# Kernel tuning notes

Measured on AMD Instinct MI355X. Metric: run time of the kernel, lower is better.

The kernel has to match this reference:

```python
import jax, jax.numpy as jnp
import numpy as np

N_NODES = 50000


def gcn_conv(x, src, dst, W, b, n):
    # PyG GCNConv: h = x @ W; out[i] = sum_j norm_ij * h[j] + b, with added self-loops
    h = x @ W  # [N, out]
    deg = jax.ops.segment_sum(jnp.ones_like(dst, dtype=h.dtype), dst, num_segments=n)
    inv_sqrt_deg = jnp.where(deg > 0, jax.lax.rsqrt(deg), 0.0)  # [N]
    coeff = inv_sqrt_deg[src] * inv_sqrt_deg[dst]  # [E]
    msg = h[src] * coeff[:, None]  # [E, out] gather (memory-bound)
    out = jax.ops.segment_sum(msg, dst, num_segments=n)  # scatter-add
    return out + b


def setup_inputs() -> dict:
    key = jax.random.key(0)
    ks = jax.random.split(key, 8)
    n, e, c_in, c_hid, c_out = N_NODES, 800000, 128, 128, 64
    x = jax.random.normal(ks[0], (n, c_in), dtype=jnp.float32)
    edge_index = jax.random.randint(ks[1], (2, e), 0, n, dtype=jnp.int64)
    # Glorot-ish scaled weights
    W1 = jax.random.normal(ks[2], (c_in, c_hid), dtype=jnp.float32) / np.sqrt(c_in)
    b1 = jnp.zeros((c_hid,), dtype=jnp.float32)
    W2 = jax.random.normal(ks[3], (c_hid, c_out), dtype=jnp.float32) / np.sqrt(c_hid)
    b2 = jnp.zeros((c_out,), dtype=jnp.float32)
    lin_W = jax.random.normal(ks[4], (2 * c_out, c_out), dtype=jnp.float32) / np.sqrt(2 * c_out)
    lin_b = jnp.zeros((c_out,), dtype=jnp.float32)
    return {"x": x, "edge_index": edge_index, "W1": W1, "b1": b1,
            "W2": W2, "b2": b2, "lin_W": lin_W, "lin_b": lin_b}


def reference(x, edge_index, W1, b1, W2, b2, lin_W, lin_b):
    n = x.shape[0]
    # add self-loops (as GCNConv does by default)
    loops = jnp.arange(n, dtype=edge_index.dtype)
    src = jnp.concatenate([edge_index[0], loops])
    dst = jnp.concatenate([edge_index[1], loops])

    def branch(x):
        h = jax.nn.relu(gcn_conv(x, src, dst, W1, b1, n))
        # dropout: identity in eval mode (training=False)
        return gcn_conv(h, src, dst, W2, b2, n)

    x1 = branch(x)
    x2 = branch(x)
    # FusionMethod == 'Concat'
    fused = jnp.concatenate([x1, x2], axis=1) @ lin_W + lin_b
    return jax.nn.log_softmax(fused, axis=1)
```

## Files before the change

kernel.cpp:

```cpp
#include <hip/hip_runtime.h>


#define CIN  128
#define CHID 128
#define COUT 64
#define BCAP_SH 13
#define BINCHUNK 2048
#define CELLCAP 32
#define ENTCAP  5120

typedef short v8s __attribute__((ext_vector_type(8)));
typedef float v4f __attribute__((ext_vector_type(4)));

static __device__ __forceinline__ unsigned short f2bf(float f) {
    unsigned int u = __float_as_uint(f);
    unsigned int r = (u + 0x7fffu + ((u >> 16) & 1u)) >> 16;
    return (unsigned short)r;
}
static __device__ __forceinline__ float bflo(unsigned int u) {
    return __uint_as_float(u << 16);
}
static __device__ __forceinline__ float bfhi(unsigned int u) {
    return __uint_as_float(u & 0xffff0000u);
}
static __device__ __forceinline__ unsigned int pk2(float a, float b) {
    return (unsigned int)f2bf(a) | ((unsigned int)f2bf(b) << 16);
}

__global__ __launch_bounds__(256) void bin_wprep_kernel(
        const int* __restrict__ src, const int* __restrict__ dst,
        int* __restrict__ cnt, unsigned int* __restrict__ binned, int E, int nchunk,
        const float* __restrict__ W1, const float* __restrict__ W2,
        const float* __restrict__ b2, const float* __restrict__ linW,
        const float* __restrict__ linb, unsigned short* __restrict__ Wt1,
        unsigned short* __restrict__ Wt2, float* __restrict__ bp) {
    int bb = blockIdx.x;
    int t = threadIdx.x;
    if (bb < nchunk) {
        __shared__ int h[256];
        __shared__ int cur[256];
        h[t] = 0;
        __syncthreads();
        int e0 = bb * BINCHUNK;
        int e1 = e0 + BINCHUNK; if (e1 > E) e1 = E;
        for (int e = e0 + t; e < e1; e += 256)
            atomicAdd(&h[dst[e] >> 8], 1);
        __syncthreads();
        int c = h[t];
        cnt[bb * 256 + t] = c < CELLCAP ? c : CELLCAP;
        cur[t] = 0;
        __syncthreads();
        for (int e = e0 + t; e < e1; e += 256) {
            int d = dst[e];
            int b = d >> 8;
            int pos = atomicAdd(&cur[b], 1);
            if (pos < CELLCAP)
                binned[((size_t)(bb * 256 + b)) * CELLCAP + pos] =
                    (unsigned int)src[e] | (((unsigned int)d & 255u) << 16);
        }
    } else {
        int wb = bb - nchunk;
        if (wb < CHID) {
            if (t < 128) {
                Wt1[wb * CIN + t] = f2bf(W1[t * CHID + wb]);
                if (t < COUT) {
                    float acc = 0.f;
#pragma unroll 8
                    for (int k = 0; k < COUT; ++k) {
                        float wsv = linW[k * COUT + t] + linW[(k + COUT) * COUT + t];
                        acc = fmaf(W2[wb * COUT + k], wsv, acc);
                    }
                    Wt2[t * CHID + wb] = f2bf(acc);
                }
            }
        } else {
            if (t < COUT) {
                float acc = 0.f;
#pragma unroll 8
                for (int k = 0; k < COUT; ++k) {
                    float wsv = linW[k * COUT + t] + linW[(k + COUT) * COUT + t];
                    acc = fmaf(b2[k], wsv, acc);
                }
                bp[t] = acc + linb[t];
            }
        }
    }
}

__global__ __launch_bounds__(512) void csr_gemm1_kernel(
        const unsigned int* __restrict__ binned, const int* __restrict__ cnt,
        int nchunk, int nbkt,
        int2* __restrict__ rowpair, float* __restrict__ inv,
        unsigned short* __restrict__ ebuf16,
        const float* __restrict__ x, const unsigned short* __restrict__ Wt1,
        unsigned short* __restrict__ h1t, int n) {
    int t = threadIdx.x;
    if ((int)blockIdx.x < nbkt) {
        int b = blockIdx.x;
        __shared__ int cc[512];
        __shared__ int ps[512];
        __shared__ unsigned int ent[ENTCAP];
        __shared__ int h[256];
        __shared__ int s2[256];
        int v = (t < nchunk) ? cnt[t * 256 + b] : 0;
        cc[t] = v;
        ps[t] = v;
        __syncthreads();
        for (int off = 1; off < 512; off <<= 1) {
            int u = (t >= off) ? ps[t - off] : 0;
            __syncthreads();
            ps[t] += u;
            __syncthreads();
        }
        int total = ps[511];
        if (total > ENTCAP) total = ENTCAP;
        if (t < nchunk && v > 0) {
            int basei = ps[t] - v;
            const unsigned int* cell = binned + ((size_t)(t * 256 + b)) * CELLCAP;
            for (int i = 0; i < v; ++i)
                if (basei + i < ENTCAP) ent[basei + i] = cell[i];
        }
        if (t < 256) h[t] = 0;
        __syncthreads();
        for (int i = t; i < total; i += 512)
            atomicAdd(&h[ent[i] >> 16], 1);
        __syncthreads();
        int myc = (t < 256) ? h[t] : 0;
        if (t < 256) s2[t] = myc;
        __syncthreads();
        for (int off = 1; off < 256; off <<= 1) {
            int u = (t >= off && t < 256) ? s2[t - off] : 0;
            __syncthreads();
            if (t < 256) s2[t] += u;
            __syncthreads();
        }
        int base = b << BCAP_SH;
        if (t < 256) {
            int excl = s2[t] - myc;
            int node = (b << 8) + t;
            if (node < n) {
                rowpair[node] = make_int2(base + excl, base + excl + myc);
                inv[node] = rsqrtf((float)(myc + 1));
            }
            h[t] = base + excl;
        }
        __syncthreads();
        for (int i = t; i < total; i += 512) {
            unsigned int e = ent[i];
            int pos = atomicAdd(&h[e >> 16], 1);
            ebuf16[pos] = (unsigned short)(e & 0xffffu);
        }
    } else {
        int bid = blockIdx.x - nbkt;
        int lane = t & 63, wave = t >> 6;
        int quad = lane >> 4, r16 = lane & 15;
        int row0 = (bid * 8 + wave) * 16;
        if (row0 >= n) return;
        int arow = row0 + r16;
        if (arow >= n) arow = n - 1;
        size_t n32 = (size_t)n * 32;

        v4f acc[8];
#pragma unroll
        for (int c = 0; c < 8; ++c) acc[c] = (v4f){0.f, 0.f, 0.f, 0.f};
#pragma unroll
        for (int kc = 0; kc < 4; ++kc) {
            const float4* ap = (const float4*)(x + (size_t)arow * 128 + kc * 32 + quad * 8);
            float4 a0 = ap[0], a1 = ap[1];
            v8s af;
            af[0] = (short)f2bf(a0.x); af[1] = (short)f2bf(a0.y);
            af[2] = (short)f2bf(a0.z); af[3] = (short)f2bf(a0.w);
            af[4] = (short)f2bf(a1.x); af[5] = (short)f2bf(a1.y);
            af[6] = (short)f2bf(a1.z); af[7] = (short)f2bf(a1.w);
#pragma unroll
            for (int ct = 0; ct < 8; ++ct) {
                v8s bf = *(const v8s*)(Wt1 + (size_t)(ct * 16 + r16) * 128 + kc * 32 + quad * 8);
                acc[ct] = __builtin_amdgcn_mfma_f32_16x16x32_bf16(af, bf, acc[ct], 0, 0, 0);
            }
        }
#pragma unroll
        for (int ct = 0; ct < 8; ++ct) {
            int col = ct * 16 + r16;
            int pl = col >> 5, d = col & 31;
#pragma unroll
            for (int i = 0; i < 4; ++i) {
                int orow = row0 + quad * 4 + i;
                if (orow < n)
                    h1t[(size_t)pl * n32 + (size_t)orow * 32 + d] = f2bf(acc[ct][i]);
            }
        }
    }
}

__global__ __launch_bounds__(256) void agg1_slice_kernel(
        const unsigned short* __restrict__ h1t,
        const unsigned short* __restrict__ ebuf16,
        const int2* __restrict__ rowpair,
        const float* __restrict__ inv,
        const float* __restrict__ b1,
        unsigned int* __restrict__ agg1b,
        int n) {
    int b = blockIdx.x;
    int xcd = b & 7;
    int slice = xcd >> 1;
    int sub = xcd & 1;
    int grp = b >> 3;
    int wid = threadIdx.x >> 6;
    int lane = threadIdx.x & 63;
    int g = lane >> 3, s = lane & 7;
    const uint2* __restrict__ plane = (const uint2*)(h1t + (size_t)slice * n * 32);

    int node = (grp * 2 + sub) * 32 + wid * 8 + g;
    int cnode = node < n ? node : n - 1;
    int2 rp = rowpair[cnode];
    int beg = rp.x, len = rp.y - rp.x;
    int m = len < 64 ? len : 64;
    uint2 usl = plane[(size_t)cnode * 8 + s];
    float wd = inv[cnode];
    float4 bv = ((const float4*)b1)[slice * 8 + s];

    int kmax = (m + 1) & ~1;
    float a0 = 0.f, a1 = 0.f, a2 = 0.f, a3 = 0.f;
    int g8 = g << 3;
    int eid = 0;
    for (int k = 0; k < kmax; k += 2) {
        if ((k & 7) == 0) eid = (int)ebuf16[beg + k + s];
        int sa = __shfl(eid, g8 + (k & 7), 64);
        int sb = __shfl(eid, g8 + (k & 7) + 1, 64);
        sb = (k + 1 < m) ? sb : cnode;
        float iva = inv[sa], ivb = inv[sb];
        uint2 ua = plane[(size_t)sa * 8 + s];
        uint2 ub = plane[(size_t)sb * 8 + s];
        a0 = fmaf(iva, bflo(ua.x), a0); a1 = fmaf(iva, bfhi(ua.x), a1);
        a2 = fmaf(iva, bflo(ua.y), a2); a3 = fmaf(iva, bfhi(ua.y), a3);
        a0 = fmaf(ivb, bflo(ub.x), a0); a1 = fmaf(ivb, bfhi(ub.x), a1);
        a2 = fmaf(ivb, bflo(ub.y), a2); a3 = fmaf(ivb, bfhi(ub.y), a3);
    }
    if (len > 64) {
        for (int k = 64; k < len; ++k) {
            int sid = (int)ebuf16[beg + k];
            float iv2 = inv[sid];
            uint2 u = plane[(size_t)sid * 8 + s];
            a0 = fmaf(iv2, bflo(u.x), a0); a1 = fmaf(iv2, bfhi(u.x), a1);
            a2 = fmaf(iv2, bflo(u.y), a2); a3 = fmaf(iv2, bfhi(u.y), a3);
        }
    }
    float c2 = (1.0f - (float)(kmax - m)) * wd;
    a0 = fmaf(c2, bflo(usl.x), a0); a1 = fmaf(c2, bfhi(usl.x), a1);
    a2 = fmaf(c2, bflo(usl.y), a2); a3 = fmaf(c2, bfhi(usl.y), a3);
    float o0 = fmaxf(fmaf(wd, a0, bv.x), 0.f);
    float o1 = fmaxf(fmaf(wd, a1, bv.y), 0.f);
    float o2 = fmaxf(fmaf(wd, a2, bv.z), 0.f);
    float o3 = fmaxf(fmaf(wd, a3, bv.w), 0.f);
    if (node < n) {
        uint2 w; w.x = pk2(o0, o1); w.y = pk2(o2, o3);
        ((uint2*)agg1b)[(size_t)node * 32 + slice * 8 + s] = w;
    }
}

__global__ __launch_bounds__(256) void gemm2_kernel(const unsigned short* __restrict__ A,
                                                    const unsigned short* __restrict__ Wt,
                                                    const float* __restrict__ inv,
                                                    unsigned short* __restrict__ h2t, int n) {
    int lane = threadIdx.x & 63;
    int wave = threadIdx.x >> 6;
    int quad = lane >> 4, r16 = lane & 15;
    int row0 = (blockIdx.x * 4 + wave) * 16;
    if (row0 >= n) return;
    int arow = row0 + r16;
    if (arow >= n) arow = n - 1;

    v4f acc[4];
#pragma unroll
    for (int c = 0; c < 4; ++c) acc[c] = (v4f){0.f, 0.f, 0.f, 0.f};
#pragma unroll
    for (int kc = 0; kc < 4; ++kc) {
        v8s af = *(const v8s*)(A + (size_t)arow * 128 + kc * 32 + quad * 8);
#pragma unroll
        for (int ct = 0; ct < 4; ++ct) {
            v8s bf = *(const v8s*)(Wt + (size_t)(ct * 16 + r16) * 128 + kc * 32 + quad * 8);
            acc[ct] = __builtin_amdgcn_mfma_f32_16x16x32_bf16(af, bf, acc[ct], 0, 0, 0);
        }
    }
    float4 iv = ((const float4*)(inv + row0))[quad];
#pragma unroll
    for (int ct = 0; ct < 4; ++ct) {
#pragma unroll
        for (int i = 0; i < 4; ++i) {
            int orow = row0 + quad * 4 + i;
            if (orow < n) {
                float sc = (i == 0) ? iv.x : (i == 1) ? iv.y : (i == 2) ? iv.z : iv.w;
                h2t[(size_t)orow * 64 + ct * 16 + r16] = f2bf(acc[ct][i] * sc);
            }
        }
    }
}

__global__ __launch_bounds__(256) void agg2_softmax_kernel(
        const unsigned short* __restrict__ h2t,
        const unsigned short* __restrict__ ebuf16,
        const int2* __restrict__ rowpair,
        const float* __restrict__ inv,
        const float* __restrict__ bp,
        float* __restrict__ outp, int n) {
    int wid = threadIdx.x >> 6;
    int lane = threadIdx.x & 63;
    int g = lane >> 3, s = lane & 7;
    int node = blockIdx.x * 32 + wid * 8 + g;
    int cnode = node < n ? node : n - 1;
    int2 rp = rowpair[cnode];
    int beg = rp.x, len = rp.y - rp.x;
    int m = len < 64 ? len : 64;
    const uint4* __restrict__ rows = (const uint4*)h2t;
    uint4 usl = rows[(size_t)cnode * 8 + s];
    float wd = inv[cnode];

    int kmax = (m + 1) & ~1;
    float a0 = 0.f, a1 = 0.f, a2 = 0.f, a3 = 0.f;
    float a4 = 0.f, a5 = 0.f, a6 = 0.f, a7 = 0.f;
    int g8 = g << 3;
    int eid = 0;
    for (int k = 0; k < kmax; k += 2) {
        if ((k & 7) == 0) eid = (int)ebuf16[beg + k + s];
        int sa = __shfl(eid, g8 + (k & 7), 64);
        int sb = __shfl(eid, g8 + (k & 7) + 1, 64);
        sb = (k + 1 < m) ? sb : cnode;
        uint4 ua = rows[(size_t)sa * 8 + s];
        uint4 ub = rows[(size_t)sb * 8 + s];
        a0 += bflo(ua.x); a1 += bfhi(ua.x); a2 += bflo(ua.y); a3 += bfhi(ua.y);
        a4 += bflo(ua.z); a5 += bfhi(ua.z); a6 += bflo(ua.w); a7 += bfhi(ua.w);
        a0 += bflo(ub.x); a1 += bfhi(ub.x); a2 += bflo(ub.y); a3 += bfhi(ub.y);
        a4 += bflo(ub.z); a5 += bfhi(ub.z); a6 += bflo(ub.w); a7 += bfhi(ub.w);
    }
    if (len > 64) {
        for (int k = 64; k < len; ++k) {
            int sid = (int)ebuf16[beg + k];
            uint4 u = rows[(size_t)sid * 8 + s];
            a0 += bflo(u.x); a1 += bfhi(u.x); a2 += bflo(u.y); a3 += bfhi(u.y);
            a4 += bflo(u.z); a5 += bfhi(u.z); a6 += bflo(u.w); a7 += bfhi(u.w);
        }
    }
    float c2 = 1.0f - (float)(kmax - m);
    a0 = fmaf(c2, bflo(usl.x), a0); a1 = fmaf(c2, bfhi(usl.x), a1);
    a2 = fmaf(c2, bflo(usl.y), a2); a3 = fmaf(c2, bfhi(usl.y), a3);
    a4 = fmaf(c2, bflo(usl.z), a4); a5 = fmaf(c2, bfhi(usl.z), a5);
    a6 = fmaf(c2, bflo(usl.w), a6); a7 = fmaf(c2, bfhi(usl.w), a7);
    float4 bpa = ((const float4*)bp)[s * 2];
    float4 bpb = ((const float4*)bp)[s * 2 + 1];
    float f0 = fmaf(wd, a0, bpa.x), f1 = fmaf(wd, a1, bpa.y);
    float f2 = fmaf(wd, a2, bpa.z), f3 = fmaf(wd, a3, bpa.w);
    float f4 = fmaf(wd, a4, bpb.x), f5 = fmaf(wd, a5, bpb.y);
    float f6 = fmaf(wd, a6, bpb.z), f7 = fmaf(wd, a7, bpb.w);
    float mx = fmaxf(fmaxf(fmaxf(f0, f1), fmaxf(f2, f3)),
                     fmaxf(fmaxf(f4, f5), fmaxf(f6, f7)));
    mx = fmaxf(mx, __shfl_xor(mx, 1, 64));
    mx = fmaxf(mx, __shfl_xor(mx, 2, 64));
    mx = fmaxf(mx, __shfl_xor(mx, 4, 64));
    float sum = expf(f0 - mx) + expf(f1 - mx) + expf(f2 - mx) + expf(f3 - mx)
              + expf(f4 - mx) + expf(f5 - mx) + expf(f6 - mx) + expf(f7 - mx);
    sum += __shfl_xor(sum, 1, 64);
    sum += __shfl_xor(sum, 2, 64);
    sum += __shfl_xor(sum, 4, 64);
    float ls = mx + logf(sum);
    if (node < n) {
        float4 w0 = make_float4(f0 - ls, f1 - ls, f2 - ls, f3 - ls);
        float4 w1 = make_float4(f4 - ls, f5 - ls, f6 - ls, f7 - ls);
        ((float4*)outp)[(size_t)node * 16 + s * 2]     = w0;
        ((float4*)outp)[(size_t)node * 16 + s * 2 + 1] = w1;
    }
}

static inline size_t align16(size_t x) { return (x + 15) & ~(size_t)15; }

extern "C" void kernel_launch(void* const* d_in, const int* in_sizes, int n_in,
                              void* d_out, int out_size, void* d_ws, size_t ws_size,
                              hipStream_t stream) {
    const float* x    = (const float*)d_in[0];
    const int*   eidx = (const int*)d_in[1];
    const float* W1   = (const float*)d_in[2];
    const float* b1   = (const float*)d_in[3];
    const float* W2   = (const float*)d_in[4];
    const float* b2   = (const float*)d_in[5];
    const float* linW = (const float*)d_in[6];
    const float* linb = (const float*)d_in[7];
    float* out = (float*)d_out;

    const int n = in_sizes[0] / CIN;
    const int E = in_sizes[1] / 2;
    const int* src = eidx;
    const int* dst = eidx + E;
    const int NBKT = (n + 255) >> 8;
    const int NCHUNK = (E + BINCHUNK - 1) / BINCHUNK;

    char* ws = (char*)d_ws;
    size_t off = 0;
    int2*  rowpair = (int2*)(ws + off);  off = align16(off + (size_t)n * 8);
    float* inv     = (float*)(ws + off); off = align16(off + (size_t)n * 4);
    int*   cnt     = (int*)(ws + off);   off = align16(off + (size_t)NCHUNK * 256 * 4);
    unsigned short* Wt1 = (unsigned short*)(ws + off); off = align16(off + (size_t)CHID * CIN * 2);
    unsigned short* Wt2 = (unsigned short*)(ws + off); off = align16(off + (size_t)COUT * CHID * 2);
    float* bp      = (float*)(ws + off); off = align16(off + (size_t)COUT * 4);
    unsigned int* binned = (unsigned int*)(ws + off);
    off = align16(off + (size_t)NCHUNK * 256 * CELLCAP * 4);
    unsigned short* ebuf16 = (unsigned short*)(ws + off);
    off = align16(off + (size_t)256 * (1 << BCAP_SH) * 2);
    unsigned short* h1t   = (unsigned short*)(ws + off); off = align16(off + (size_t)n * CHID * 2);
    unsigned int*   agg1b = (unsigned int*)(ws + off);   off = align16(off + (size_t)n * CHID * 2);
    unsigned short* h2t   = (unsigned short*)(ws + off); off = align16(off + (size_t)n * COUT * 2);

    bin_wprep_kernel<<<NCHUNK + CHID + 1, 256, 0, stream>>>(
        src, dst, cnt, binned, E, NCHUNK, W1, W2, b2, linW, linb, Wt1, Wt2, bp);

    const int G1B = (n + 127) / 128;
    csr_gemm1_kernel<<<NBKT + G1B, 512, 0, stream>>>(
        binned, cnt, NCHUNK, NBKT, rowpair, inv, ebuf16, x, Wt1, h1t, n);

    const int NG1 = (n + 63) / 64;
    agg1_slice_kernel<<<NG1 * 8, 256, 0, stream>>>(h1t, ebuf16, rowpair, inv, b1, agg1b, n);

    gemm2_kernel<<<(n + 63) / 64, 256, 0, stream>>>((const unsigned short*)agg1b, Wt2, inv, h2t, n);

    agg2_softmax_kernel<<<(n + 31) / 32, 256, 0, stream>>>(h2t, ebuf16, rowpair, inv, bp, out, n);
}
```

Baseline: 191.6 us.

## Merge all stages into one cooperative persistent kernel with grid syncs

Replaces the five separate kernel launches with a single cooperative mega-kernel. Each stage runs as a grid-strided loop, and stages are separated by grid-wide barriers. The CSR build no longer stages entries in a large shared buffer and reads binned cells straight from global memory. Aggregation 2 is split from the log-softmax pass, which now goes through the output buffer. The aim is to remove launch overhead and the tail gaps between kernels. In exchange it adds several grid syncs, occupancy limits from the persistent grid, and an extra round trip of the output through global memory.

```diff
diff --git a/kernel.cpp b/kernel.cpp
--- a/kernel.cpp
+++ b/kernel.cpp
@@ -1,4 +1,7 @@
 #include <hip/hip_runtime.h>
+#include <hip/hip_cooperative_groups.h>
+
+namespace cg = cooperative_groups;
 
 
 #define CIN  128
@@ -7,7 +10,6 @@
 #define BCAP_SH 13
 #define BINCHUNK 2048
 #define CELLCAP 32
-#define ENTCAP  5120
 
 typedef short v8s __attribute__((ext_vector_type(8)));
 typedef float v4f __attribute__((ext_vector_type(4)));
@@ -27,346 +29,345 @@
     return (unsigned int)f2bf(a) | ((unsigned int)f2bf(b) << 16);
 }
 
-__global__ __launch_bounds__(256) void bin_wprep_kernel(
-        const int* __restrict__ src, const int* __restrict__ dst,
-        int* __restrict__ cnt, unsigned int* __restrict__ binned, int E, int nchunk,
-        const float* __restrict__ W1, const float* __restrict__ W2,
-        const float* __restrict__ b2, const float* __restrict__ linW,
-        const float* __restrict__ linb, unsigned short* __restrict__ Wt1,
-        unsigned short* __restrict__ Wt2, float* __restrict__ bp) {
-    int bb = blockIdx.x;
-    int t = threadIdx.x;
-    if (bb < nchunk) {
-        __shared__ int h[256];
-        __shared__ int cur[256];
-        h[t] = 0;
-        __syncthreads();
-        int e0 = bb * BINCHUNK;
-        int e1 = e0 + BINCHUNK; if (e1 > E) e1 = E;
-        for (int e = e0 + t; e < e1; e += 256)
-            atomicAdd(&h[dst[e] >> 8], 1);
-        __syncthreads();
-        int c = h[t];
-        cnt[bb * 256 + t] = c < CELLCAP ? c : CELLCAP;
-        cur[t] = 0;
-        __syncthreads();
-        for (int e = e0 + t; e < e1; e += 256) {
-            int d = dst[e];
-            int b = d >> 8;
-            int pos = atomicAdd(&cur[b], 1);
-            if (pos < CELLCAP)
-                binned[((size_t)(bb * 256 + b)) * CELLCAP + pos] =
-                    (unsigned int)src[e] | (((unsigned int)d & 255u) << 16);
-        }
-    } else {
-        int wb = bb - nchunk;
-        if (wb < CHID) {
-            if (t < 128) {
-                Wt1[wb * CIN + t] = f2bf(W1[t * CHID + wb]);
-                if (t < COUT) {
-                    float acc = 0.f;
+struct MP {
+    const int* src; const int* dst;
+    const float* W1; const float* b1; const float* W2; const float* b2;
+    const float* linW; const float* linb; const float* x;
+    int* cnt; unsigned int* binned;
+    unsigned short* Wt1; unsigned short* Wt2; float* bp;
+    int2* rowpair; float* inv; unsigned short* ebuf16;
+    unsigned short* h1t; unsigned short* agg1b; unsigned short* h2t;
+    float* out;
+    int E, n, nchunk, nbkt;
+};
+
+__global__ __launch_bounds__(256, 4) void mega_kernel(MP p) {
+    cg::grid_group gg = cg::this_grid();
+    __shared__ int shA[256];
+    __shared__ int shB[256];
+    const int t = threadIdx.x;
+    const int nb = gridDim.x;
+    const int lane = t & 63;
+    const int wid = t >> 6;
+    const size_t n32 = (size_t)p.n * 32;
+
+    for (int u = blockIdx.x; u < p.nchunk + CHID + 1; u += nb) {
+        if (u < p.nchunk) {
+            shA[t] = 0;
+            __syncthreads();
+            int e0 = u * BINCHUNK;
+            int e1 = e0 + BINCHUNK; if (e1 > p.E) e1 = p.E;
+            for (int e = e0 + t; e < e1; e += 256)
+                atomicAdd(&shA[p.dst[e] >> 8], 1);
+            __syncthreads();
+            int c = shA[t];
+            p.cnt[u * 256 + t] = c < CELLCAP ? c : CELLCAP;
+            shB[t] = 0;
+            __syncthreads();
+            for (int e = e0 + t; e < e1; e += 256) {
+                int d = p.dst[e];
+                int b = d >> 8;
+                int pos = atomicAdd(&shB[b], 1);
+                if (pos < CELLCAP)
+                    p.binned[((size_t)(u * 256 + b)) * CELLCAP + pos] =
+                        (unsigned int)p.src[e] | (((unsigned int)d & 255u) << 16);
+            }
+            __syncthreads();
+        } else {
+            int wb = u - p.nchunk;
+            if (wb < CHID) {
+                if (t < 128) {
+                    p.Wt1[wb * CIN + t] = f2bf(p.W1[t * CHID + wb]);
+                    if (t < COUT) {
+                        float acc = 0.f;
 #pragma unroll 8
-                    for (int k = 0; k < COUT; ++k) {
-                        float wsv = linW[k * COUT + t] + linW[(k + COUT) * COUT + t];
-                        acc = fmaf(W2[wb * COUT + k], wsv, acc);
+                        for (int k = 0; k < COUT; ++k) {
+                            float wsv = p.linW[k * COUT + t] + p.linW[(k + COUT) * COUT + t];
+                            acc = fmaf(p.W2[wb * COUT + k], wsv, acc);
+                        }
+                        p.Wt2[t * CHID + wb] = f2bf(acc);
                     }
-                    Wt2[t * CHID + wb] = f2bf(acc);
-                }
-            }
-        } else {
-            if (t < COUT) {
+                }
+            } else if (t < COUT) {
                 float acc = 0.f;
 #pragma unroll 8
                 for (int k = 0; k < COUT; ++k) {
-                    float wsv = linW[k * COUT + t] + linW[(k + COUT) * COUT + t];
-                    acc = fmaf(b2[k], wsv, acc);
-                }
-                bp[t] = acc + linb[t];
-            }
-        }
-    }
-}
-
-__global__ __launch_bounds__(512) void csr_gemm1_kernel(
-        const unsigned int* __restrict__ binned, const int* __restrict__ cnt,
-        int nchunk, int nbkt,
-        int2* __restrict__ rowpair, float* __restrict__ inv,
-        unsigned short* __restrict__ ebuf16,
-        const float* __restrict__ x, const unsigned short* __restrict__ Wt1,
-        unsigned short* __restrict__ h1t, int n) {
-    int t = threadIdx.x;
-    if ((int)blockIdx.x < nbkt) {
-        int b = blockIdx.x;
-        __shared__ int cc[512];
-        __shared__ int ps[512];
-        __shared__ unsigned int ent[ENTCAP];
-        __shared__ int h[256];
-        __shared__ int s2[256];
-        int v = (t < nchunk) ? cnt[t * 256 + b] : 0;
-        cc[t] = v;
-        ps[t] = v;
-        __syncthreads();
-        for (int off = 1; off < 512; off <<= 1) {
-            int u = (t >= off) ? ps[t - off] : 0;
-            __syncthreads();
-            ps[t] += u;
-            __syncthreads();
-        }
-        int total = ps[511];
-        if (total > ENTCAP) total = ENTCAP;
-        if (t < nchunk && v > 0) {
-            int basei = ps[t] - v;
-            const unsigned int* cell = binned + ((size_t)(t * 256 + b)) * CELLCAP;
-            for (int i = 0; i < v; ++i)
-                if (basei + i < ENTCAP) ent[basei + i] = cell[i];
-        }
-        if (t < 256) h[t] = 0;
-        __syncthreads();
-        for (int i = t; i < total; i += 512)
-            atomicAdd(&h[ent[i] >> 16], 1);
-        __syncthreads();
-        int myc = (t < 256) ? h[t] : 0;
-        if (t < 256) s2[t] = myc;
+                    float wsv = p.linW[k * COUT + t] + p.linW[(k + COUT) * COUT + t];
+                    acc = fmaf(p.b2[k], wsv, acc);
+                }
+                p.bp[t] = acc + p.linb[t];
+            }
+        }
+    }
+    gg.sync();
+
+    for (int b = blockIdx.x; b < p.nbkt; b += nb) {
+        shA[t] = 0;
+        __syncthreads();
+        for (int c = t; c < p.nchunk; c += 256) {
+            int cc = p.cnt[c * 256 + b];
+            const unsigned int* cell = p.binned + ((size_t)(c * 256 + b)) * CELLCAP;
+            for (int i = 0; i < cc; ++i)
+                atomicAdd(&shA[cell[i] >> 16], 1);
+        }
+        __syncthreads();
+        int myc = shA[t];
+        shB[t] = myc;
         __syncthreads();
         for (int off = 1; off < 256; off <<= 1) {
-            int u = (t >= off && t < 256) ? s2[t - off] : 0;
-            __syncthreads();
-            if (t < 256) s2[t] += u;
+            int v = (t >= off) ? shB[t - off] : 0;
+            __syncthreads();
+            shB[t] += v;
             __syncthreads();
         }
         int base = b << BCAP_SH;
-        if (t < 256) {
-            int excl = s2[t] - myc;
-            int node = (b << 8) + t;
-            if (node < n) {
-                rowpair[node] = make_int2(base + excl, base + excl + myc);
-                inv[node] = rsqrtf((float)(myc + 1));
-            }
-            h[t] = base + excl;
-        }
-        __syncthreads();
-        for (int i = t; i < total; i += 512) {
-            unsigned int e = ent[i];
-            int pos = atomicAdd(&h[e >> 16], 1);
-            ebuf16[pos] = (unsigned short)(e & 0xffffu);
-        }
-    } else {
-        int bid = blockIdx.x - nbkt;
-        int lane = t & 63, wave = t >> 6;
+        int excl = shB[t] - myc;
+        int node = (b << 8) + t;
+        if (node < p.n) {
+            p.rowpair[node] = make_int2(base + excl, base + excl + myc);
+            p.inv[node] = rsqrtf((float)(myc + 1));
+        }
+        __syncthreads();
+        shA[t] = base + excl;
+        __syncthreads();
+        for (int c = t; c < p.nchunk; c += 256) {
+            int cc = p.cnt[c * 256 + b];
+            const unsigned int* cell = p.binned + ((size_t)(c * 256 + b)) * CELLCAP;
+            for (int i = 0; i < cc; ++i) {
+                unsigned int e = cell[i];
+                int pos = atomicAdd(&shA[e >> 16], 1);
+                p.ebuf16[pos] = (unsigned short)(e & 0xffffu);
+            }
+        }
+        __syncthreads();
+    }
+    gg.sync();
+
+    {
         int quad = lane >> 4, r16 = lane & 15;
-        int row0 = (bid * 8 + wave) * 16;
-        if (row0 >= n) return;
-        int arow = row0 + r16;
-        if (arow >= n) arow = n - 1;
-        size_t n32 = (size_t)n * 32;
-
-        v4f acc[8];
-#pragma unroll
-        for (int c = 0; c < 8; ++c) acc[c] = (v4f){0.f, 0.f, 0.f, 0.f};
-#pragma unroll
-        for (int kc = 0; kc < 4; ++kc) {
-            const float4* ap = (const float4*)(x + (size_t)arow * 128 + kc * 32 + quad * 8);
-            float4 a0 = ap[0], a1 = ap[1];
-            v8s af;
-            af[0] = (short)f2bf(a0.x); af[1] = (short)f2bf(a0.y);
-            af[2] = (short)f2bf(a0.z); af[3] = (short)f2bf(a0.w);
-            af[4] = (short)f2bf(a1.x); af[5] = (short)f2bf(a1.y);
-            af[6] = (short)f2bf(a1.z); af[7] = (short)f2bf(a1.w);
+        int nunits = (p.n + 63) >> 6;
+        for (int u = blockIdx.x; u < nunits; u += nb) {
+            int row0 = u * 64 + wid * 16;
+            if (row0 >= p.n) continue;
+            int arow = row0 + r16;
+            if (arow >= p.n) arow = p.n - 1;
+            v4f acc[8];
+#pragma unroll
+            for (int c = 0; c < 8; ++c) acc[c] = (v4f){0.f, 0.f, 0.f, 0.f};
+#pragma unroll
+            for (int kc = 0; kc < 4; ++kc) {
+                const float4* ap = (const float4*)(p.x + (size_t)arow * 128 + kc * 32 + quad * 8);
+                float4 a0 = ap[0], a1 = ap[1];
+                v8s af;
+                af[0] = (short)f2bf(a0.x); af[1] = (short)f2bf(a0.y);
+                af[2] = (short)f2bf(a0.z); af[3] = (short)f2bf(a0.w);
+                af[4] = (short)f2bf(a1.x); af[5] = (short)f2bf(a1.y);
+                af[6] = (short)f2bf(a1.z); af[7] = (short)f2bf(a1.w);
+#pragma unroll
+                for (int ct = 0; ct < 8; ++ct) {
+                    v8s bf = *(const v8s*)(p.Wt1 + (size_t)(ct * 16 + r16) * 128 + kc * 32 + quad * 8);
+                    acc[ct] = __builtin_amdgcn_mfma_f32_16x16x32_bf16(af, bf, acc[ct], 0, 0, 0);
+                }
+            }
+            float4 iv = ((const float4*)(p.inv + row0))[quad];
 #pragma unroll
             for (int ct = 0; ct < 8; ++ct) {
-                v8s bf = *(const v8s*)(Wt1 + (size_t)(ct * 16 + r16) * 128 + kc * 32 + quad * 8);
-                acc[ct] = __builtin_amdgcn_mfma_f32_16x16x32_bf16(af, bf, acc[ct], 0, 0, 0);
-            }
-        }
-#pragma unroll
-        for (int ct = 0; ct < 8; ++ct) {
-            int col = ct * 16 + r16;
-            int pl = col >> 5, d = col & 31;
-#pragma unroll
-            for (int i = 0; i < 4; ++i) {
-                int orow = row0 + quad * 4 + i;
-                if (orow < n)
-                    h1t[(size_t)pl * n32 + (size_t)orow * 32 + d] = f2bf(acc[ct][i]);
-            }
-        }
-    }
-}
-
-__global__ __launch_bounds__(256) void agg1_slice_kernel(
-        const unsigned short* __restrict__ h1t,
-        const unsigned short* __restrict__ ebuf16,
-        const int2* __restrict__ rowpair,
-        const float* __restrict__ inv,
-        const float* __restrict__ b1,
-        unsigned int* __restrict__ agg1b,
-        int n) {
-    int b = blockIdx.x;
-    int xcd = b & 7;
-    int slice = xcd >> 1;
-    int sub = xcd & 1;
-    int grp = b >> 3;
-    int wid = threadIdx.x >> 6;
-    int lane = threadIdx.x & 63;
-    int g = lane >> 3, s = lane & 7;
-    const uint2* __restrict__ plane = (const uint2*)(h1t + (size_t)slice * n * 32);
-
-    int node = (grp * 2 + sub) * 32 + wid * 8 + g;
-    int cnode = node < n ? node : n - 1;
-    int2 rp = rowpair[cnode];
-    int beg = rp.x, len = rp.y - rp.x;
-    int m = len < 64 ? len : 64;
-    uint2 usl = plane[(size_t)cnode * 8 + s];
-    float wd = inv[cnode];
-    float4 bv = ((const float4*)b1)[slice * 8 + s];
-
-    int kmax = (m + 1) & ~1;
-    float a0 = 0.f, a1 = 0.f, a2 = 0.f, a3 = 0.f;
-    int g8 = g << 3;
-    int eid = 0;
-    for (int k = 0; k < kmax; k += 2) {
-        if ((k & 7) == 0) eid = (int)ebuf16[beg + k + s];
-        int sa = __shfl(eid, g8 + (k & 7), 64);
-        int sb = __shfl(eid, g8 + (k & 7) + 1, 64);
-        sb = (k + 1 < m) ? sb : cnode;
-        float iva = inv[sa], ivb = inv[sb];
-        uint2 ua = plane[(size_t)sa * 8 + s];
-        uint2 ub = plane[(size_t)sb * 8 + s];
-        a0 = fmaf(iva, bflo(ua.x), a0); a1 = fmaf(iva, bfhi(ua.x), a1);
-        a2 = fmaf(iva, bflo(ua.y), a2); a3 = fmaf(iva, bfhi(ua.y), a3);
-        a0 = fmaf(ivb, bflo(ub.x), a0); a1 = fmaf(ivb, bfhi(ub.x), a1);
-        a2 = fmaf(ivb, bflo(ub.y), a2); a3 = fmaf(ivb, bfhi(ub.y), a3);
-    }
-    if (len > 64) {
-        for (int k = 64; k < len; ++k) {
-            int sid = (int)ebuf16[beg + k];
-            float iv2 = inv[sid];
-            uint2 u = plane[(size_t)sid * 8 + s];
-            a0 = fmaf(iv2, bflo(u.x), a0); a1 = fmaf(iv2, bfhi(u.x), a1);
-            a2 = fmaf(iv2, bflo(u.y), a2); a3 = fmaf(iv2, bfhi(u.y), a3);
-        }
-    }
-    float c2 = (1.0f - (float)(kmax - m)) * wd;
-    a0 = fmaf(c2, bflo(usl.x), a0); a1 = fmaf(c2, bfhi(usl.x), a1);
-    a2 = fmaf(c2, bflo(usl.y), a2); a3 = fmaf(c2, bfhi(usl.y), a3);
-    float o0 = fmaxf(fmaf(wd, a0, bv.x), 0.f);
-    float o1 = fmaxf(fmaf(wd, a1, bv.y), 0.f);
-    float o2 = fmaxf(fmaf(wd, a2, bv.z), 0.f);
-    float o3 = fmaxf(fmaf(wd, a3, bv.w), 0.f);
-    if (node < n) {
-        uint2 w; w.x = pk2(o0, o1); w.y = pk2(o2, o3);
-        ((uint2*)agg1b)[(size_t)node * 32 + slice * 8 + s] = w;
-    }
-}
-
-__global__ __launch_bounds__(256) void gemm2_kernel(const unsigned short* __restrict__ A,
-                                                    const unsigned short* __restrict__ Wt,
-                                                    const float* __restrict__ inv,
-                                                    unsigned short* __restrict__ h2t, int n) {
-    int lane = threadIdx.x & 63;
-    int wave = threadIdx.x >> 6;
-    int quad = lane >> 4, r16 = lane & 15;
-    int row0 = (blockIdx.x * 4 + wave) * 16;
-    if (row0 >= n) return;
-    int arow = row0 + r16;
-    if (arow >= n) arow = n - 1;
-
-    v4f acc[4];
-#pragma unroll
-    for (int c = 0; c < 4; ++c) acc[c] = (v4f){0.f, 0.f, 0.f, 0.f};
-#pragma unroll
-    for (int kc = 0; kc < 4; ++kc) {
-        v8s af = *(const v8s*)(A + (size_t)arow * 128 + kc * 32 + quad * 8);
-#pragma unroll
-        for (int ct = 0; ct < 4; ++ct) {
-            v8s bf = *(const v8s*)(Wt + (size_t)(ct * 16 + r16) * 128 + kc * 32 + quad * 8);
-            acc[ct] = __builtin_amdgcn_mfma_f32_16x16x32_bf16(af, bf, acc[ct], 0, 0, 0);
-        }
-    }
-    float4 iv = ((const float4*)(inv + row0))[quad];
-#pragma unroll
-    for (int ct = 0; ct < 4; ++ct) {
-#pragma unroll
-        for (int i = 0; i < 4; ++i) {
-            int orow = row0 + quad * 4 + i;
-            if (orow < n) {
-                float sc = (i == 0) ? iv.x : (i == 1) ? iv.y : (i == 2) ? iv.z : iv.w;
-                h2t[(size_t)orow * 64 + ct * 16 + r16] = f2bf(acc[ct][i] * sc);
-            }
-        }
-    }
-}
-
-__global__ __launch_bounds__(256) void agg2_softmax_kernel(
-        const unsigned short* __restrict__ h2t,
-        const unsigned short* __restrict__ ebuf16,
-        const int2* __restrict__ rowpair,
-        const float* __restrict__ inv,
-        const float* __restrict__ bp,
-        float* __restrict__ outp, int n) {
-    int wid = threadIdx.x >> 6;
-    int lane = threadIdx.x & 63;
-    int g = lane >> 3, s = lane & 7;
-    int node = blockIdx.x * 32 + wid * 8 + g;
-    int cnode = node < n ? node : n - 1;
-    int2 rp = rowpair[cnode];
-    int beg = rp.x, len = rp.y - rp.x;
-    int m = len < 64 ? len : 64;
-    const uint4* __restrict__ rows = (const uint4*)h2t;
-    uint4 usl = rows[(size_t)cnode * 8 + s];
-    float wd = inv[cnode];
-
-    int kmax = (m + 1) & ~1;
-    float a0 = 0.f, a1 = 0.f, a2 = 0.f, a3 = 0.f;
-    float a4 = 0.f, a5 = 0.f, a6 = 0.f, a7 = 0.f;
-    int g8 = g << 3;
-    int eid = 0;
-    for (int k = 0; k < kmax; k += 2) {
-        if ((k & 7) == 0) eid = (int)ebuf16[beg + k + s];
-        int sa = __shfl(eid, g8 + (k & 7), 64);
-        int sb = __shfl(eid, g8 + (k & 7) + 1, 64);
-        sb = (k + 1 < m) ? sb : cnode;
-        uint4 ua = rows[(size_t)sa * 8 + s];
-        uint4 ub = rows[(size_t)sb * 8 + s];
-        a0 += bflo(ua.x); a1 += bfhi(ua.x); a2 += bflo(ua.y); a3 += bfhi(ua.y);
-        a4 += bflo(ua.z); a5 += bfhi(ua.z); a6 += bflo(ua.w); a7 += bfhi(ua.w);
-        a0 += bflo(ub.x); a1 += bfhi(ub.x); a2 += bflo(ub.y); a3 += bfhi(ub.y);
-        a4 += bflo(ub.z); a5 += bfhi(ub.z); a6 += bflo(ub.w); a7 += bfhi(ub.w);
-    }
-    if (len > 64) {
-        for (int k = 64; k < len; ++k) {
-            int sid = (int)ebuf16[beg + k];
-            uint4 u = rows[(size_t)sid * 8 + s];
-            a0 += bflo(u.x); a1 += bfhi(u.x); a2 += bflo(u.y); a3 += bfhi(u.y);
-            a4 += bflo(u.z); a5 += bfhi(u.z); a6 += bflo(u.w); a7 += bfhi(u.w);
-        }
-    }
-    float c2 = 1.0f - (float)(kmax - m);
-    a0 = fmaf(c2, bflo(usl.x), a0); a1 = fmaf(c2, bfhi(usl.x), a1);
-    a2 = fmaf(c2, bflo(usl.y), a2); a3 = fmaf(c2, bfhi(usl.y), a3);
-    a4 = fmaf(c2, bflo(usl.z), a4); a5 = fmaf(c2, bfhi(usl.z), a5);
-    a6 = fmaf(c2, bflo(usl.w), a6); a7 = fmaf(c2, bfhi(usl.w), a7);
-    float4 bpa = ((const float4*)bp)[s * 2];
-    float4 bpb = ((const float4*)bp)[s * 2 + 1];
-    float f0 = fmaf(wd, a0, bpa.x), f1 = fmaf(wd, a1, bpa.y);
-    float f2 = fmaf(wd, a2, bpa.z), f3 = fmaf(wd, a3, bpa.w);
-    float f4 = fmaf(wd, a4, bpb.x), f5 = fmaf(wd, a5, bpb.y);
-    float f6 = fmaf(wd, a6, bpb.z), f7 = fmaf(wd, a7, bpb.w);
-    float mx = fmaxf(fmaxf(fmaxf(f0, f1), fmaxf(f2, f3)),
-                     fmaxf(fmaxf(f4, f5), fmaxf(f6, f7)));
-    mx = fmaxf(mx, __shfl_xor(mx, 1, 64));
-    mx = fmaxf(mx, __shfl_xor(mx, 2, 64));
-    mx = fmaxf(mx, __shfl_xor(mx, 4, 64));
-    float sum = expf(f0 - mx) + expf(f1 - mx) + expf(f2 - mx) + expf(f3 - mx)
-              + expf(f4 - mx) + expf(f5 - mx) + expf(f6 - mx) + expf(f7 - mx);
-    sum += __shfl_xor(sum, 1, 64);
-    sum += __shfl_xor(sum, 2, 64);
-    sum += __shfl_xor(sum, 4, 64);
-    float ls = mx + logf(sum);
-    if (node < n) {
-        float4 w0 = make_float4(f0 - ls, f1 - ls, f2 - ls, f3 - ls);
-        float4 w1 = make_float4(f4 - ls, f5 - ls, f6 - ls, f7 - ls);
-        ((float4*)outp)[(size_t)node * 16 + s * 2]     = w0;
-        ((float4*)outp)[(size_t)node * 16 + s * 2 + 1] = w1;
+                int col = ct * 16 + r16;
+                int pl = col >> 5, d = col & 31;
+#pragma unroll
+                for (int i = 0; i < 4; ++i) {
+                    int orow = row0 + quad * 4 + i;
+                    if (orow < p.n) {
+                        float sc = (i == 0) ? iv.x : (i == 1) ? iv.y : (i == 2) ? iv.z : iv.w;
+                        p.h1t[(size_t)pl * n32 + (size_t)orow * 32 + d] = f2bf(acc[ct][i] * sc);
+                    }
+                }
+            }
+        }
+    }
+    gg.sync();
+
+    {
+        int g = lane >> 3, s = lane & 7;
+        int g8 = g << 3;
+        int nunits = ((p.n + 63) >> 6) * 8;
+        for (int u = blockIdx.x; u < nunits; u += nb) {
+            int xcd = u & 7, slice = xcd >> 1, sub = xcd & 1, grp = u >> 3;
+            const uint2* plane = (const uint2*)(p.h1t + (size_t)slice * p.n * 32);
+            int node = (grp * 2 + sub) * 32 + wid * 8 + g;
+            int cnode = node < p.n ? node : p.n - 1;
+            int2 rp = p.rowpair[cnode];
+            int beg = rp.x, len = rp.y - rp.x;
+            int m = len < 64 ? len : 64;
+            uint2 usl = plane[(size_t)cnode * 8 + s];
+            float wd = p.inv[cnode];
+            float4 bv = ((const float4*)p.b1)[slice * 8 + s];
+            int kmax = (m + 3) & ~3;
+            float a0 = 0.f, a1 = 0.f, a2 = 0.f, a3 = 0.f;
+            int eid = 0;
+            for (int k = 0; k < kmax; k += 4) {
+                if ((k & 7) == 0) eid = (int)p.ebuf16[beg + k + s];
+                int i0 = __shfl(eid, g8 + (k & 7) + 0, 64);
+                int i1 = __shfl(eid, g8 + (k & 7) + 1, 64);
+                int i2 = __shfl(eid, g8 + (k & 7) + 2, 64);
+                int i3 = __shfl(eid, g8 + (k & 7) + 3, 64);
+                i0 = (k     < m) ? i0 : cnode;
+                i1 = (k + 1 < m) ? i1 : cnode;
+                i2 = (k + 2 < m) ? i2 : cnode;
+                i3 = (k + 3 < m) ? i3 : cnode;
+                uint2 u0 = plane[(size_t)i0 * 8 + s];
+                uint2 u1 = plane[(size_t)i1 * 8 + s];
+                uint2 u2 = plane[(size_t)i2 * 8 + s];
+                uint2 u3 = plane[(size_t)i3 * 8 + s];
+                a0 += bflo(u0.x); a1 += bfhi(u0.x); a2 += bflo(u0.y); a3 += bfhi(u0.y);
+                a0 += bflo(u1.x); a1 += bfhi(u1.x); a2 += bflo(u1.y); a3 += bfhi(u1.y);
+                a0 += bflo(u2.x); a1 += bfhi(u2.x); a2 += bflo(u2.y); a3 += bfhi(u2.y);
+                a0 += bflo(u3.x); a1 += bfhi(u3.x); a2 += bflo(u3.y); a3 += bfhi(u3.y);
+            }
+            if (len > 64) {
+                for (int k = 64; k < len; ++k) {
+                    int sid = (int)p.ebuf16[beg + k];
+                    uint2 uu = plane[(size_t)sid * 8 + s];
+                    a0 += bflo(uu.x); a1 += bfhi(uu.x); a2 += bflo(uu.y); a3 += bfhi(uu.y);
+                }
+            }
+            float cc = 1.0f - (float)(kmax - m);
+            a0 = fmaf(cc, bflo(usl.x), a0); a1 = fmaf(cc, bfhi(usl.x), a1);
+            a2 = fmaf(cc, bflo(usl.y), a2); a3 = fmaf(cc, bfhi(usl.y), a3);
+            float o0 = fmaxf(fmaf(wd, a0, bv.x), 0.f);
+            float o1 = fmaxf(fmaf(wd, a1, bv.y), 0.f);
+            float o2 = fmaxf(fmaf(wd, a2, bv.z), 0.f);
+            float o3 = fmaxf(fmaf(wd, a3, bv.w), 0.f);
+            if (node < p.n) {
+                uint2 w; w.x = pk2(o0, o1); w.y = pk2(o2, o3);
+                ((uint2*)p.agg1b)[(size_t)node * 32 + slice * 8 + s] = w;
+            }
+        }
+    }
+    gg.sync();
+
+    {
+        int quad = lane >> 4, r16 = lane & 15;
+        int nunits = (p.n + 63) >> 6;
+        for (int u = blockIdx.x; u < nunits; u += nb) {
+            int row0 = u * 64 + wid * 16;
+            if (row0 >= p.n) continue;
+            int arow = row0 + r16;
+            if (arow >= p.n) arow = p.n - 1;
+            v4f acc[4];
+#pragma unroll
+            for (int c = 0; c < 4; ++c) acc[c] = (v4f){0.f, 0.f, 0.f, 0.f};
+#pragma unroll
+            for (int kc = 0; kc < 4; ++kc) {
+                v8s af = *(const v8s*)(p.agg1b + (size_t)arow * 128 + kc * 32 + quad * 8);
+#pragma unroll
+                for (int ct = 0; ct < 4; ++ct) {
+                    v8s bf = *(const v8s*)(p.Wt2 + (size_t)(ct * 16 + r16) * 128 + kc * 32 + quad * 8);
+                    acc[ct] = __builtin_amdgcn_mfma_f32_16x16x32_bf16(af, bf, acc[ct], 0, 0, 0);
+                }
+            }
+            float4 iv = ((const float4*)(p.inv + row0))[quad];
+#pragma unroll
+            for (int ct = 0; ct < 4; ++ct) {
+                int col = ct * 16 + r16;
+                int pl = col >> 5, d = col & 31;
+#pragma unroll
+                for (int i = 0; i < 4; ++i) {
+                    int orow = row0 + quad * 4 + i;
+                    if (orow < p.n) {
+                        float sc = (i == 0) ? iv.x : (i == 1) ? iv.y : (i == 2) ? iv.z : iv.w;
+                        p.h2t[(size_t)pl * n32 + (size_t)orow * 32 + d] = f2bf(acc[ct][i] * sc);
+                    }
+                }
+            }
+        }
+    }
+    gg.sync();
+
+    {
+        int g = lane >> 3, s = lane & 7;
+        int g8 = g << 3;
+        int nunits = ((p.n + 127) >> 7) * 8;
+        for (int u = blockIdx.x; u < nunits; u += nb) {
+            int xcd = u & 7, slice = xcd >> 2, sub = xcd & 3, grp = u >> 3;
+            const uint2* plane = (const uint2*)(p.h2t + (size_t)slice * p.n * 32);
+            int node = (grp * 4 + sub) * 32 + wid * 8 + g;
+            int cnode = node < p.n ? node : p.n - 1;
+            int2 rp = p.rowpair[cnode];
+            int beg = rp.x, len = rp.y - rp.x;
+            int m = len < 64 ? len : 64;
+            uint2 usl = plane[(size_t)cnode * 8 + s];
+            float wd = p.inv[cnode];
+            float4 bpv = ((const float4*)p.bp)[slice * 8 + s];
+            int kmax = (m + 3) & ~3;
+            float a0 = 0.f, a1 = 0.f, a2 = 0.f, a3 = 0.f;
+            int eid = 0;
+            for (int k = 0; k < kmax; k += 4) {
+                if ((k & 7) == 0) eid = (int)p.ebuf16[beg + k + s];
+                int i0 = __shfl(eid, g8 + (k & 7) + 0, 64);
+                int i1 = __shfl(eid, g8 + (k & 7) + 1, 64);
+                int i2 = __shfl(eid, g8 + (k & 7) + 2, 64);
+                int i3 = __shfl(eid, g8 + (k & 7) + 3, 64);
+                i0 = (k     < m) ? i0 : cnode;
+                i1 = (k + 1 < m) ? i1 : cnode;
+                i2 = (k + 2 < m) ? i2 : cnode;
+                i3 = (k + 3 < m) ? i3 : cnode;
+                uint2 u0 = plane[(size_t)i0 * 8 + s];
+                uint2 u1 = plane[(size_t)i1 * 8 + s];
+                uint2 u2 = plane[(size_t)i2 * 8 + s];
+                uint2 u3 = plane[(size_t)i3 * 8 + s];
+                a0 += bflo(u0.x); a1 += bfhi(u0.x); a2 += bflo(u0.y); a3 += bfhi(u0.y);
+                a0 += bflo(u1.x); a1 += bfhi(u1.x); a2 += bflo(u1.y); a3 += bfhi(u1.y);
+                a0 += bflo(u2.x); a1 += bfhi(u2.x); a2 += bflo(u2.y); a3 += bfhi(u2.y);
+                a0 += bflo(u3.x); a1 += bfhi(u3.x); a2 += bflo(u3.y); a3 += bfhi(u3.y);
+            }
+            if (len > 64) {
+                for (int k = 64; k < len; ++k) {
+                    int sid = (int)p.ebuf16[beg + k];
+                    uint2 uu = plane[(size_t)sid * 8 + s];
+                    a0 += bflo(uu.x); a1 += bfhi(uu.x); a2 += bflo(uu.y); a3 += bfhi(uu.y);
+                }
+            }
+            float cc = 1.0f - (float)(kmax - m);
+            a0 = fmaf(cc, bflo(usl.x), a0); a1 = fmaf(cc, bfhi(usl.x), a1);
+            a2 = fmaf(cc, bflo(usl.y), a2); a3 = fmaf(cc, bfhi(usl.y), a3);
+            if (node < p.n) {
+                float4 w;
+                w.x = fmaf(wd, a0, bpv.x);
+                w.y = fmaf(wd, a1, bpv.y);
+                w.z = fmaf(wd, a2, bpv.z);
+                w.w = fmaf(wd, a3, bpv.w);
+                ((float4*)p.out)[(size_t)node * 16 + slice * 8 + s] = w;
+            }
+        }
+    }
+    gg.sync();
+
+    {
+        int g = lane >> 3, s = lane & 7;
+        int nunits = (p.n + 31) >> 5;
+        for (int u = blockIdx.x; u < nunits; u += nb) {
+            int node = u * 32 + wid * 8 + g;
+            int cnode = node < p.n ? node : p.n - 1;
+            float4 va = ((const float4*)p.out)[(size_t)cnode * 16 + s * 2];
+            float4 vb = ((const float4*)p.out)[(size_t)cnode * 16 + s * 2 + 1];
+            float mx = fmaxf(fmaxf(fmaxf(va.x, va.y), fmaxf(va.z, va.w)),
+                             fmaxf(fmaxf(vb.x, vb.y), fmaxf(vb.z, vb.w)));
+            mx = fmaxf(mx, __shfl_xor(mx, 1, 64));
+            mx = fmaxf(mx, __shfl_xor(mx, 2, 64));
+            mx = fmaxf(mx, __shfl_xor(mx, 4, 64));
+            float sm = expf(va.x - mx) + expf(va.y - mx) + expf(va.z - mx) + expf(va.w - mx)
+                     + expf(vb.x - mx) + expf(vb.y - mx) + expf(vb.z - mx) + expf(vb.w - mx);
+            sm += __shfl_xor(sm, 1, 64);
+            sm += __shfl_xor(sm, 2, 64);
+            sm += __shfl_xor(sm, 4, 64);
+            float ls = mx + logf(sm);
+            if (node < p.n) {
+                float4* orow = (float4*)p.out + (size_t)node * 16;
+                orow[s * 2]     = make_float4(va.x - ls, va.y - ls, va.z - ls, va.w - ls);
+                orow[s * 2 + 1] = make_float4(vb.x - ls, vb.y - ls, vb.z - ls, vb.w - ls);
+            }
+        }
     }
 }
 
@@ -387,8 +388,6 @@
 
     const int n = in_sizes[0] / CIN;
     const int E = in_sizes[1] / 2;
-    const int* src = eidx;
-    const int* dst = eidx + E;
     const int NBKT = (n + 255) >> 8;
     const int NCHUNK = (E + BINCHUNK - 1) / BINCHUNK;
 
@@ -405,20 +404,24 @@
     unsigned short* ebuf16 = (unsigned short*)(ws + off);
     off = align16(off + (size_t)256 * (1 << BCAP_SH) * 2);
     unsigned short* h1t   = (unsigned short*)(ws + off); off = align16(off + (size_t)n * CHID * 2);
-    unsigned int*   agg1b = (unsigned int*)(ws + off);   off = align16(off + (size_t)n * CHID * 2);
+    unsigned short* agg1b = (unsigned short*)(ws + off); off = align16(off + (size_t)n * CHID * 2);
     unsigned short* h2t   = (unsigned short*)(ws + off); off = align16(off + (size_t)n * COUT * 2);
 
-    bin_wprep_kernel<<<NCHUNK + CHID + 1, 256, 0, stream>>>(
-        src, dst, cnt, binned, E, NCHUNK, W1, W2, b2, linW, linb, Wt1, Wt2, bp);
-
-    const int G1B = (n + 127) / 128;
-    csr_gemm1_kernel<<<NBKT + G1B, 512, 0, stream>>>(
-        binned, cnt, NCHUNK, NBKT, rowpair, inv, ebuf16, x, Wt1, h1t, n);
-
-    const int NG1 = (n + 63) / 64;
-    agg1_slice_kernel<<<NG1 * 8, 256, 0, stream>>>(h1t, ebuf16, rowpair, inv, b1, agg1b, n);
-
-    gemm2_kernel<<<(n + 63) / 64, 256, 0, stream>>>((const unsigned short*)agg1b, Wt2, inv, h2t, n);
-
-    agg2_softmax_kernel<<<(n + 31) / 32, 256, 0, stream>>>(h2t, ebuf16, rowpair, inv, bp, out, n);
-}
+    MP p;
+    p.src = eidx; p.dst = eidx + E;
+    p.W1 = W1; p.b1 = b1; p.W2 = W2; p.b2 = b2; p.linW = linW; p.linb = linb; p.x = x;
+    p.cnt = cnt; p.binned = binned; p.Wt1 = Wt1; p.Wt2 = Wt2; p.bp = bp;
+    p.rowpair = rowpair; p.inv = inv; p.ebuf16 = ebuf16;
+    p.h1t = h1t; p.agg1b = agg1b; p.h2t = h2t; p.out = out;
+    p.E = E; p.n = n; p.nchunk = NCHUNK; p.nbkt = NBKT;
+
+    int maxb = 0;
+    hipOccupancyMaxActiveBlocksPerMultiprocessor(&maxb, mega_kernel, 256, 0);
+    int nblk = maxb * 256;
+    if (nblk > 1024) nblk = 1024;
+    nblk &= ~7;
+    if (nblk < 8) nblk = 8;
+
+    void* kargs[] = { (void*)&p };
+    hipLaunchCooperativeKernel(mega_kernel, dim3(nblk), dim3(256), kargs, 0, stream);
+}
```

New measurement: 620.7 us. 3.24x slower.
